# Performance work log

Measured on AMD Instinct MI355X. Metric: run time of the kernel, lower is better.

## Reference

```python
import jax, jax.numpy as jnp
from jax import lax
import numpy as np

EPS = 1e-5


def adder2d(x, w):
    """AdderNet 'conv': out[b,o,h,w] = -sum_{c,kh,kw} |x_patch - w[o,c,kh,kw]|, stride 1, VALID."""
    O, C, K, _ = w.shape
    # patches: [B, C*K*K, H', W'], feature dim ordered (c, kh, kw) matching w.reshape(O, -1)
    patches = lax.conv_general_dilated_patches(x, (K, K), (1, 1), 'VALID')
    wf = w.reshape(O, C * K * K)
    # broadcast: [B, O, CKK, H', W'] -> reduce CKK
    d = jnp.abs(patches[:, None, :, :, :] - wf[None, :, :, None, None])
    return -d.sum(axis=2)


def batchnorm(x, gamma, beta):
    # training-mode BatchNorm2d: batch statistics over (N, H, W), biased variance
    mean = x.mean(axis=(0, 2, 3), keepdims=True)
    var = x.var(axis=(0, 2, 3), keepdims=True)
    inv = lax.rsqrt(var + EPS)
    return gamma[None, :, None, None] * (x - mean) * inv + beta[None, :, None, None]


def maxpool2x2(x):
    return lax.reduce_window(x, -jnp.inf, lax.max, (1, 1, 2, 2), (1, 1, 2, 2), 'VALID')


def setup_inputs() -> dict:
    key = jax.random.key(0)
    ks = jax.random.split(key, 8)
    B = 128
    x = jax.random.normal(ks[0], (B, 1, 28, 28), dtype=jnp.float32)
    w1 = jax.random.normal(ks[1], (20, 1, 5, 5), dtype=jnp.float32) * 0.2
    w2 = jax.random.normal(ks[2], (50, 20, 5, 5), dtype=jnp.float32) * 0.063  # ~1/sqrt(500)
    gamma1 = jnp.ones((20,), jnp.float32)
    beta1 = jnp.zeros((20,), jnp.float32)
    gamma2 = jnp.ones((50,), jnp.float32)
    beta2 = jnp.zeros((50,), jnp.float32)
    fc1_w = jax.random.normal(ks[3], (500, 800), dtype=jnp.float32) * 0.035
    fc1_b = jnp.zeros((500,), jnp.float32)
    fc2_w = jax.random.normal(ks[4], (10, 500), dtype=jnp.float32) * 0.045
    fc2_b = jnp.zeros((10,), jnp.float32)
    return {"x": x, "w1": w1, "gamma1": gamma1, "beta1": beta1,
            "w2": w2, "gamma2": gamma2, "beta2": beta2,
            "fc1_w": fc1_w, "fc1_b": fc1_b, "fc2_w": fc2_w, "fc2_b": fc2_b}


def reference(x, w1, gamma1, beta1, w2, gamma2, beta2, fc1_w, fc1_b, fc2_w, fc2_b):
    h = adder2d(x, w1)                 # [B,20,24,24]
    h = batchnorm(h, gamma1, beta1)
    h = maxpool2x2(h)                  # [B,20,12,12]
    h = adder2d(h, w2)                 # [B,50,8,8]
    h = batchnorm(h, gamma2, beta2)
    h = maxpool2x2(h)                  # [B,50,4,4]
    h = h.reshape(h.shape[0], 800)
    h = jax.nn.relu(h @ fc1_w.T + fc1_b)
    logits = h @ fc2_w.T + fc2_b       # [B,10]
    return jax.nn.softmax(logits, axis=1)
```

## Files before the change

### kernel.cpp

```cpp
#include <hip/hip_runtime.h>
#include <hip/hip_bf16.h>
#include <math.h>


#define B_N 128
#define EPSBN 1e-5f
#define NCOPY 16

__global__ __launch_bounds__(256) void adder1_bn_kernel(
    const float* __restrict__ x, const float* __restrict__ w1,
    float* __restrict__ out, float* __restrict__ sums) {
  __shared__ float csum[40];
  if (threadIdx.x < 40) csum[threadIdx.x] = 0.f;
  __syncthreads();
  int idx = blockIdx.x * 256 + threadIdx.x;
  int owc = idx % 3; int t = idx / 3;
  int oh  = t % 24;  t /= 24;
  int o   = t % 20;  int b = t / 20;
  const float* xb = x + b * 784;
  const float* wb = w1 + o * 25;
  float acc[8];
#pragma unroll
  for (int i = 0; i < 8; ++i) acc[i] = 0.f;
#pragma unroll
  for (int kh = 0; kh < 5; ++kh) {
    float xr[12];
    const float4* xp = (const float4*)(xb + (oh + kh) * 28 + owc * 8);
#pragma unroll
    for (int i = 0; i < 3; ++i) {
      float4 v = xp[i];
      xr[4*i] = v.x; xr[4*i+1] = v.y; xr[4*i+2] = v.z; xr[4*i+3] = v.w;
    }
    float wr[5];
#pragma unroll
    for (int i = 0; i < 5; ++i) wr[i] = wb[kh * 5 + i];
#pragma unroll
    for (int ow = 0; ow < 8; ++ow)
#pragma unroll
      for (int kw = 0; kw < 5; ++kw)
        acc[ow] += fabsf(xr[ow + kw] - wr[kw]);
  }
  float* op = out + (((size_t)b * 20 + o) * 24 + oh) * 24 + owc * 8;
  float4 s0 = { -acc[0], -acc[1], -acc[2], -acc[3] };
  float4 s1 = { -acc[4], -acc[5], -acc[6], -acc[7] };
  *(float4*)(op)     = s0;
  *(float4*)(op + 4) = s1;
  float s = 0.f, s2 = 0.f;
#pragma unroll
  for (int i = 0; i < 8; ++i) { s -= acc[i]; s2 += acc[i] * acc[i]; }
  atomicAdd(&csum[o * 2],     s);
  atomicAdd(&csum[o * 2 + 1], s2);
  __syncthreads();
  if (threadIdx.x < 40) {
    float v = csum[threadIdx.x];
    if (v != 0.f)
      atomicAdd(&sums[(blockIdx.x & (NCOPY - 1)) * 40 + threadIdx.x], v);
  }
}

__global__ __launch_bounds__(256) void bn_pool_kernel(
    const float* __restrict__ h, const float* __restrict__ sums, int stride,
    const float* __restrict__ gamma, const float* __restrict__ beta,
    float* __restrict__ out, int C, int Hin, int Hout, float inv_n) {
  int idx = blockIdx.x * 256 + threadIdx.x;
  int pw = idx % Hout; int t = idx / Hout;
  int ph = t % Hout;   t /= Hout;
  int c  = t % C;      int b = t / C;
  float sm = 0.f, s2 = 0.f;
#pragma unroll
  for (int cp = 0; cp < NCOPY; ++cp) {
    sm += sums[cp * stride + 2 * c];
    s2 += sums[cp * stride + 2 * c + 1];
  }
  float mean = sm * inv_n;
  float var  = s2 * inv_n - mean * mean;
  float sc   = gamma[c] * rsqrtf(var + EPSBN);
  float bi   = beta[c] - mean * sc;
  const float* hp = h + ((b * C + c) * Hin + 2 * ph) * Hin + 2 * pw;
  float2 r0 = *(const float2*)(hp);
  float2 r1 = *(const float2*)(hp + Hin);
  float v0 = fmaf(sc, r0.x, bi);
  float v1 = fmaf(sc, r0.y, bi);
  float v2 = fmaf(sc, r1.x, bi);
  float v3 = fmaf(sc, r1.y, bi);
  out[idx] = fmaxf(fmaxf(v0, v1), fmaxf(v2, v3));
}

__global__ __launch_bounds__(256) void bn_pool_t_kernel(
    const float* __restrict__ h, const float* __restrict__ sums,
    const float* __restrict__ gamma, const float* __restrict__ beta,
    float* __restrict__ outT, float inv_n) {
  int idx = blockIdx.x * 256 + threadIdx.x;
  int pw = idx % 4; int t = idx / 4;
  int ph = t % 4;   t /= 4;
  int c  = t % 50;  int b = t / 50;
  float sm = 0.f, s2 = 0.f;
#pragma unroll
  for (int cp = 0; cp < NCOPY; ++cp) {
    sm += sums[cp * 100 + 2 * c];
    s2 += sums[cp * 100 + 2 * c + 1];
  }
  float mean = sm * inv_n;
  float var  = s2 * inv_n - mean * mean;
  float sc   = gamma[c] * rsqrtf(var + EPSBN);
  float bi   = beta[c] - mean * sc;
  const float* hp = h + ((b * 50 + c) * 8 + 2 * ph) * 8 + 2 * pw;
  float2 r0 = *(const float2*)(hp);
  float2 r1 = *(const float2*)(hp + 8);
  float v0 = fmaf(sc, r0.x, bi);
  float v1 = fmaf(sc, r0.y, bi);
  float v2 = fmaf(sc, r1.x, bi);
  float v3 = fmaf(sc, r1.y, bi);
  int k = (c * 16 + ph * 4 + pw);
  outT[k * 128 + b] = fmaxf(fmaxf(v0, v1), fmaxf(v2, v3));
}

__global__ __launch_bounds__(256) void w2t_prep_kernel(
    const float* __restrict__ w2, float* __restrict__ w2t) {
  int idx = blockIdx.x * 256 + threadIdx.x;
  int o = idx & 63;
  int t = idx >> 6;
  int k = t % 25, c = t / 25;
  w2t[idx] = (o < 50) ? w2[o * 500 + c * 25 + k] : 0.f;
}

__global__ __launch_bounds__(256) void adder2_bn_kernel(
    const float* __restrict__ h, const float* __restrict__ w2t,
    float* __restrict__ out, float* __restrict__ sums) {
  __shared__ float lh[1440];
  __shared__ float csum[100];
  if (threadIdx.x < 100) csum[threadIdx.x] = 0.f;
  const int oq = blockIdx.x & 3;
  const int b  = blockIdx.x >> 2;
  {
    const float* hb = h + (size_t)b * 2880 + 2 * oq * 12;
    float2* dst = (float2*)lh;
    for (int j = threadIdx.x; j < 720; j += 256) {
      int c = j / 36, rem = j - c * 36;
      dst[j] = ((const float2*)(hb + c * 144))[rem];
    }
  }
  __syncthreads();
  const int o   = threadIdx.x >> 2;
  const int q   = threadIdx.x & 3;
  const int ohl = q >> 1;
  const int owh = q & 1;
  if (o < 50) {
    float acc[4];
#pragma unroll
    for (int i = 0; i < 4; ++i) acc[i] = 0.f;
    for (int c = 0; c < 20; ++c) {
      const float* lc = lh + c * 72 + owh * 4;
      const float* wc = w2t + c * 1600 + o;
#pragma unroll
      for (int kh = 0; kh < 5; ++kh) {
        float hr[8];
        const float* lp = lc + (ohl + kh) * 12;
        *(float4*)(hr)     = *(const float4*)(lp);
        *(float4*)(hr + 4) = *(const float4*)(lp + 4);
        float wr[5];
#pragma unroll
        for (int i = 0; i < 5; ++i) wr[i] = wc[(kh * 5 + i) * 64];
#pragma unroll
        for (int ow = 0; ow < 4; ++ow)
#pragma unroll
          for (int kw = 0; kw < 5; ++kw)
            acc[ow] += fabsf(hr[ow + kw] - wr[kw]);
      }
    }
    const int oh = 2 * oq + ohl;
    float4 st = { -acc[0], -acc[1], -acc[2], -acc[3] };
    *(float4*)(out + (((size_t)b * 50 + o) * 8 + oh) * 8 + owh * 4) = st;
    float s = 0.f, s2 = 0.f;
#pragma unroll
    for (int i = 0; i < 4; ++i) { s -= acc[i]; s2 += acc[i] * acc[i]; }
    atomicAdd(&csum[o * 2],     s);
    atomicAdd(&csum[o * 2 + 1], s2);
  }
  __syncthreads();
  if (threadIdx.x < 100)
    atomicAdd(&sums[(blockIdx.x & (NCOPY - 1)) * 100 + threadIdx.x],
              csum[threadIdx.x]);
}

__global__ __launch_bounds__(256) void fc1_kernel(
    const float* __restrict__ featT, const float* __restrict__ w1,
    const float* __restrict__ b1, float* __restrict__ hid) {
  const int j = blockIdx.x;
  const int b = threadIdx.x & 127;
  const int khalf = threadIdx.x >> 7;
  const float* wr = w1 + j * 800;
  const float* fb = featT + b;
  float a0 = 0.f, a1 = 0.f, a2 = 0.f, a3 = 0.f;
  int k0 = khalf * 400;
  for (int k = k0; k < k0 + 400; k += 4) {
    float4 w4 = *(const float4*)(wr + k);
    a0 = fmaf(fb[(k    ) * 128], w4.x, a0);
    a1 = fmaf(fb[(k + 1) * 128], w4.y, a1);
    a2 = fmaf(fb[(k + 2) * 128], w4.z, a2);
    a3 = fmaf(fb[(k + 3) * 128], w4.w, a3);
  }
  __shared__ float part[256];
  part[threadIdx.x] = (a0 + a1) + (a2 + a3);
  __syncthreads();
  if (threadIdx.x < 128)
    hid[b * 512 + j] =
        fmaxf(b1[j] + part[threadIdx.x] + part[threadIdx.x + 128], 0.f);
}

__global__ __launch_bounds__(64) void fc2_softmax_kernel(
    const float* __restrict__ hid, const float* __restrict__ w2,
    const float* __restrict__ b2, float* __restrict__ out) {
  const int b = blockIdx.x, lane = threadIdx.x;
  const float* hb = hid + b * 512;
  __shared__ float logit[16];
  float hv[8];
#pragma unroll
  for (int i = 0; i < 8; ++i) {
    int k = lane + 64 * i;
    hv[i] = (k < 500) ? hb[k] : 0.f;
  }
  for (int j = 0; j < 10; ++j) {
    const float* wr = w2 + j * 500;
    float acc = 0.f;
#pragma unroll
    for (int i = 0; i < 8; ++i) {
      int k = lane + 64 * i;
      float w = (k < 500) ? wr[k] : 0.f;
      acc = fmaf(hv[i], w, acc);
    }
#pragma unroll
    for (int off = 32; off > 0; off >>= 1) acc += __shfl_down(acc, off);
    if (lane == 0) logit[j] = acc + b2[j];
  }
  __syncthreads();
  if (lane == 0) {
    float m = logit[0];
    for (int j = 1; j < 10; ++j) m = fmaxf(m, logit[j]);
    float s = 0.f, e[10];
    for (int j = 0; j < 10; ++j) { e[j] = __expf(logit[j] - m); s += e[j]; }
    float inv = 1.f / s;
    for (int j = 0; j < 10; ++j) out[b * 10 + j] = e[j] * inv;
  }
}

extern "C" void kernel_launch(void* const* d_in, const int* in_sizes, int n_in,
                              void* d_out, int out_size, void* d_ws, size_t ws_size,
                              hipStream_t stream) {
  const float* x   = (const float*)d_in[0];
  const float* w1  = (const float*)d_in[1];
  const float* g1  = (const float*)d_in[2];
  const float* be1 = (const float*)d_in[3];
  const float* w2  = (const float*)d_in[4];
  const float* g2  = (const float*)d_in[5];
  const float* be2 = (const float*)d_in[6];
  const float* fw1 = (const float*)d_in[7];
  const float* fb1 = (const float*)d_in[8];
  const float* fw2 = (const float*)d_in[9];
  const float* fb2 = (const float*)d_in[10];
  float* out = (float*)d_out;

  float* ws    = (float*)d_ws;
  float* h1    = ws;
  float* h1p   = ws + 1474560;
  float* h2    = ws;
  float* featT = ws + 409600;
  float* hid   = ws + 512000;
  float* w2t   = ws + 600000;
  float* sums1 = ws + 1843200;
  float* sums2 = sums1 + NCOPY*40;

  hipMemsetAsync(sums1, 0, NCOPY * 140 * sizeof(float), stream);

  adder1_bn_kernel<<<720, 256, 0, stream>>>(x, w1, h1, sums1);
  bn_pool_kernel<<<1440, 256, 0, stream>>>(h1, sums1, 40, g1, be1, h1p,
                                           20, 24, 12, 1.f / (B_N * 576));
  w2t_prep_kernel<<<125, 256, 0, stream>>>(w2, w2t);
  adder2_bn_kernel<<<512, 256, 0, stream>>>(h1p, w2t, h2, sums2);
  bn_pool_t_kernel<<<400, 256, 0, stream>>>(h2, sums2, g2, be2, featT,
                                            1.f / (B_N * 64));
  fc1_kernel<<<500, 256, 0, stream>>>(featT, fw1, fb1, hid);
  fc2_softmax_kernel<<<128, 64, 0, stream>>>(hid, fw2, fb2, out);
}
```

Measured before the change: 147.5 us.

## Fuse BN1+maxpool into adder2 tile load and merge weight prep with memset

The first batchnorm and 2x2 maxpool are folded into the shared-memory load of the second adder kernel, so each block computes the scale and bias from the partial sums and pools the raw adder1 output directly. This removes the separate bn_pool kernel and the h1p intermediate write and read. The w2 transpose and the zeroing of the stat buffers are merged into one prep kernel, replacing the memset and one launch. In exchange, each adder2 block redoes the BN stat reduction and reads a 4x larger slice of unpooled h1, and the workspace layout is rearranged so the buffers no longer overlap.

Result: faster. 141.8 us (-3.9%).

```diff
diff --git a/kernel.cpp b/kernel.cpp
--- a/kernel.cpp
+++ b/kernel.cpp
@@ -6,6 +6,19 @@
 #define B_N 128
 #define EPSBN 1e-5f
 #define NCOPY 16
+
+__global__ __launch_bounds__(256) void prep_kernel(
+    const float* __restrict__ w2, float* __restrict__ w2t,
+    float* __restrict__ sums) {
+  int idx = blockIdx.x * 256 + threadIdx.x;
+  if (idx < 32000) {
+    int o = idx & 63, t = idx >> 6, k = t % 25, c = t / 25;
+    w2t[idx] = (o < 50) ? w2[o * 500 + c * 25 + k] : 0.f;
+  } else {
+    int j = idx - 32000;
+    if (j < NCOPY * 140) sums[j] = 0.f;
+  }
+}
 
 __global__ __launch_bounds__(256) void adder1_bn_kernel(
     const float* __restrict__ x, const float* __restrict__ w1,
@@ -58,32 +71,92 @@
   }
 }
 
-__global__ __launch_bounds__(256) void bn_pool_kernel(
-    const float* __restrict__ h, const float* __restrict__ sums, int stride,
-    const float* __restrict__ gamma, const float* __restrict__ beta,
-    float* __restrict__ out, int C, int Hin, int Hout, float inv_n) {
-  int idx = blockIdx.x * 256 + threadIdx.x;
-  int pw = idx % Hout; int t = idx / Hout;
-  int ph = t % Hout;   t /= Hout;
-  int c  = t % C;      int b = t / C;
-  float sm = 0.f, s2 = 0.f;
-#pragma unroll
-  for (int cp = 0; cp < NCOPY; ++cp) {
-    sm += sums[cp * stride + 2 * c];
-    s2 += sums[cp * stride + 2 * c + 1];
-  }
-  float mean = sm * inv_n;
-  float var  = s2 * inv_n - mean * mean;
-  float sc   = gamma[c] * rsqrtf(var + EPSBN);
-  float bi   = beta[c] - mean * sc;
-  const float* hp = h + ((b * C + c) * Hin + 2 * ph) * Hin + 2 * pw;
-  float2 r0 = *(const float2*)(hp);
-  float2 r1 = *(const float2*)(hp + Hin);
-  float v0 = fmaf(sc, r0.x, bi);
-  float v1 = fmaf(sc, r0.y, bi);
-  float v2 = fmaf(sc, r1.x, bi);
-  float v3 = fmaf(sc, r1.y, bi);
-  out[idx] = fmaxf(fmaxf(v0, v1), fmaxf(v2, v3));
+__global__ __launch_bounds__(256) void adder2_bn_kernel(
+    const float* __restrict__ h1, const float* __restrict__ sums1,
+    const float* __restrict__ g1, const float* __restrict__ be1,
+    const float* __restrict__ w2t,
+    float* __restrict__ out, float* __restrict__ sums2) {
+  __shared__ float lh[1440];
+  __shared__ float sb[40];
+  __shared__ float csum[100];
+  const int tid = threadIdx.x;
+  if (tid < 100) csum[tid] = 0.f;
+  if (tid < 20) {
+    float sm = 0.f, s2 = 0.f;
+#pragma unroll
+    for (int cp = 0; cp < NCOPY; ++cp) {
+      sm += sums1[cp * 40 + 2 * tid];
+      s2 += sums1[cp * 40 + 2 * tid + 1];
+    }
+    const float inv_n = 1.f / (B_N * 576);
+    float mean = sm * inv_n;
+    float var  = s2 * inv_n - mean * mean;
+    float sc   = g1[tid] * rsqrtf(var + EPSBN);
+    sb[2 * tid]     = sc;
+    sb[2 * tid + 1] = be1[tid] - mean * sc;
+  }
+  __syncthreads();
+
+  const int oq = blockIdx.x & 3;
+  const int b  = blockIdx.x >> 2;
+
+  {
+    const float* hb = h1 + (size_t)b * 11520;
+    for (int j = tid; j < 1440; j += 256) {
+      int c = j / 72, rem = j - c * 72;
+      int r = rem / 12, col = rem - r * 12;
+      const float* hp = hb + (c * 24 + (4 * oq + 2 * r)) * 24 + 2 * col;
+      float2 r0 = *(const float2*)(hp);
+      float2 r1 = *(const float2*)(hp + 24);
+      float sc = sb[2 * c], bi = sb[2 * c + 1];
+      float v0 = fmaf(sc, r0.x, bi);
+      float v1 = fmaf(sc, r0.y, bi);
+      float v2 = fmaf(sc, r1.x, bi);
+      float v3 = fmaf(sc, r1.y, bi);
+      lh[j] = fmaxf(fmaxf(v0, v1), fmaxf(v2, v3));
+    }
+  }
+  __syncthreads();
+
+  const int o   = tid >> 2;
+  const int q   = tid & 3;
+  const int ohl = q >> 1;
+  const int owh = q & 1;
+  if (o < 50) {
+    float acc[4];
+#pragma unroll
+    for (int i = 0; i < 4; ++i) acc[i] = 0.f;
+    for (int c = 0; c < 20; ++c) {
+      const float* lc = lh + c * 72 + owh * 4;
+      const float* wc = w2t + c * 1600 + o;
+#pragma unroll
+      for (int kh = 0; kh < 5; ++kh) {
+        float hr[8];
+        const float* lp = lc + (ohl + kh) * 12;
+        *(float4*)(hr)     = *(const float4*)(lp);
+        *(float4*)(hr + 4) = *(const float4*)(lp + 4);
+        float wr[5];
+#pragma unroll
+        for (int i = 0; i < 5; ++i) wr[i] = wc[(kh * 5 + i) * 64];
+#pragma unroll
+        for (int ow = 0; ow < 4; ++ow)
+#pragma unroll
+          for (int kw = 0; kw < 5; ++kw)
+            acc[ow] += fabsf(hr[ow + kw] - wr[kw]);
+      }
+    }
+    const int oh = 2 * oq + ohl;
+    float4 st = { -acc[0], -acc[1], -acc[2], -acc[3] };
+    *(float4*)(out + (((size_t)b * 50 + o) * 8 + oh) * 8 + owh * 4) = st;
+    float s = 0.f, s2 = 0.f;
+#pragma unroll
+    for (int i = 0; i < 4; ++i) { s -= acc[i]; s2 += acc[i] * acc[i]; }
+    atomicAdd(&csum[o * 2],     s);
+    atomicAdd(&csum[o * 2 + 1], s2);
+  }
+  __syncthreads();
+  if (tid < 100)
+    atomicAdd(&sums2[(blockIdx.x & (NCOPY - 1)) * 100 + tid], csum[tid]);
 }
 
 __global__ __launch_bounds__(256) void bn_pool_t_kernel(
@@ -113,74 +186,6 @@
   float v3 = fmaf(sc, r1.y, bi);
   int k = (c * 16 + ph * 4 + pw);
   outT[k * 128 + b] = fmaxf(fmaxf(v0, v1), fmaxf(v2, v3));
-}
-
-__global__ __launch_bounds__(256) void w2t_prep_kernel(
-    const float* __restrict__ w2, float* __restrict__ w2t) {
-  int idx = blockIdx.x * 256 + threadIdx.x;
-  int o = idx & 63;
-  int t = idx >> 6;
-  int k = t % 25, c = t / 25;
-  w2t[idx] = (o < 50) ? w2[o * 500 + c * 25 + k] : 0.f;
-}
-
-__global__ __launch_bounds__(256) void adder2_bn_kernel(
-    const float* __restrict__ h, const float* __restrict__ w2t,
-    float* __restrict__ out, float* __restrict__ sums) {
-  __shared__ float lh[1440];
-  __shared__ float csum[100];
-  if (threadIdx.x < 100) csum[threadIdx.x] = 0.f;
-  const int oq = blockIdx.x & 3;
-  const int b  = blockIdx.x >> 2;
-  {
-    const float* hb = h + (size_t)b * 2880 + 2 * oq * 12;
-    float2* dst = (float2*)lh;
-    for (int j = threadIdx.x; j < 720; j += 256) {
-      int c = j / 36, rem = j - c * 36;
-      dst[j] = ((const float2*)(hb + c * 144))[rem];
-    }
-  }
-  __syncthreads();
-  const int o   = threadIdx.x >> 2;
-  const int q   = threadIdx.x & 3;
-  const int ohl = q >> 1;
-  const int owh = q & 1;
-  if (o < 50) {
-    float acc[4];
-#pragma unroll
-    for (int i = 0; i < 4; ++i) acc[i] = 0.f;
-    for (int c = 0; c < 20; ++c) {
-      const float* lc = lh + c * 72 + owh * 4;
-      const float* wc = w2t + c * 1600 + o;
-#pragma unroll
-      for (int kh = 0; kh < 5; ++kh) {
-        float hr[8];
-        const float* lp = lc + (ohl + kh) * 12;
-        *(float4*)(hr)     = *(const float4*)(lp);
-        *(float4*)(hr + 4) = *(const float4*)(lp + 4);
-        float wr[5];
-#pragma unroll
-        for (int i = 0; i < 5; ++i) wr[i] = wc[(kh * 5 + i) * 64];
-#pragma unroll
-        for (int ow = 0; ow < 4; ++ow)
-#pragma unroll
-          for (int kw = 0; kw < 5; ++kw)
-            acc[ow] += fabsf(hr[ow + kw] - wr[kw]);
-      }
-    }
-    const int oh = 2 * oq + ohl;
-    float4 st = { -acc[0], -acc[1], -acc[2], -acc[3] };
-    *(float4*)(out + (((size_t)b * 50 + o) * 8 + oh) * 8 + owh * 4) = st;
-    float s = 0.f, s2 = 0.f;
-#pragma unroll
-    for (int i = 0; i < 4; ++i) { s -= acc[i]; s2 += acc[i] * acc[i]; }
-    atomicAdd(&csum[o * 2],     s);
-    atomicAdd(&csum[o * 2 + 1], s2);
-  }
-  __syncthreads();
-  if (threadIdx.x < 100)
-    atomicAdd(&sums[(blockIdx.x & (NCOPY - 1)) * 100 + threadIdx.x],
-              csum[threadIdx.x]);
 }
 
 __global__ __launch_bounds__(256) void fc1_kernel(
@@ -262,21 +267,16 @@
 
   float* ws    = (float*)d_ws;
   float* h1    = ws;
-  float* h1p   = ws + 1474560;
-  float* h2    = ws;
-  float* featT = ws + 409600;
-  float* hid   = ws + 512000;
-  float* w2t   = ws + 600000;
   float* sums1 = ws + 1843200;
-  float* sums2 = sums1 + NCOPY*40;
-
-  hipMemsetAsync(sums1, 0, NCOPY * 140 * sizeof(float), stream);
-
+  float* sums2 = ws + 1843840;
+  float* w2t   = ws + 1845504;
+  float* h2    = ws + 1900000;
+  float* featT = ws + 2310000;
+  float* hid   = ws + 2420000;
+
+  prep_kernel<<<134, 256, 0, stream>>>(w2, w2t, sums1);
   adder1_bn_kernel<<<720, 256, 0, stream>>>(x, w1, h1, sums1);
-  bn_pool_kernel<<<1440, 256, 0, stream>>>(h1, sums1, 40, g1, be1, h1p,
-                                           20, 24, 12, 1.f / (B_N * 576));
-  w2t_prep_kernel<<<125, 256, 0, stream>>>(w2, w2t);
-  adder2_bn_kernel<<<512, 256, 0, stream>>>(h1p, w2t, h2, sums2);
+  adder2_bn_kernel<<<512, 256, 0, stream>>>(h1, sums1, g1, be1, w2t, h2, sums2);
   bn_pool_t_kernel<<<400, 256, 0, stream>>>(h2, sums2, g2, be2, featT,
                                             1.f / (B_N * 64));
   fc1_kernel<<<500, 256, 0, stream>>>(featT, fw1, fb1, hid);
```
